# Performance work log

Measured on AMD Instinct MI355X. Metric: run time of the kernel, lower is better.

Reference implementation:

```python
import math
import jax, jax.numpy as jnp
import numpy as np

DIM = 2048
HEAD_DIM = 64
N_HEADS = DIM // HEAD_DIM
BATCH = 4
SEQ = 1025  # 32*32 axial positions + 1 zero position
EPS = 1e-6


def make_theta(head_dim=HEAD_DIM, h=32, w=32):
    # freqs: geometric from pi to 10*pi, head_dim//4 of them
    n_freqs = head_dim // 4
    freqs = jnp.exp(jnp.linspace(math.log(math.pi), math.log(10 * math.pi), n_freqs))
    hp = jnp.linspace(-1.0, 1.0, h + 1)
    wp = jnp.linspace(-1.0, 1.0, w + 1)
    hp = (hp[:-1] + hp[1:]) / 2
    wp = (wp[:-1] + wp[1:]) / 2
    pos = jnp.stack(jnp.meshgrid(hp, wp, indexing='ij'), axis=-1).reshape(h * w, 2)
    pos = jnp.concatenate([jnp.zeros((1, 2)), pos], axis=0)  # [1025, 2]
    theta_h = pos[:, 0:1] * freqs  # [S, n_freqs]
    theta_w = pos[:, 1:2] * freqs
    return jnp.concatenate([theta_h, theta_w], axis=-1)  # [S, head_dim//2]


def rms_norm(x, scale, eps=EPS):
    mean_sq = jnp.mean(jnp.square(x.astype(jnp.float32)), axis=-1, keepdims=True)
    s = scale.astype(jnp.float32) * jax.lax.rsqrt(mean_sq + eps)
    return (x * s.astype(x.dtype)).astype(x.dtype)


def apply_rotary(x, theta):
    # x: [B, H, S, D], theta: [S, d] with 2*d <= D
    d = theta.shape[-1]
    x1, x2, x3 = x[..., :d], x[..., d:2 * d], x[..., 2 * d:]
    cos, sin = jnp.cos(theta), jnp.sin(theta)  # broadcast over B, H
    y1 = x1 * cos - x2 * sin
    y2 = x2 * cos + x1 * sin
    return jnp.concatenate([y1, y2, x3], axis=-1)


def setup_inputs() -> dict:
    key = jax.random.key(0)
    k1, k2, k3 = jax.random.split(key, 3)
    x = jax.random.normal(k1, (BATCH, SEQ, DIM), dtype=jnp.float32)
    scale = jnp.ones((DIM,), dtype=jnp.float32)
    w_qkv = jax.random.normal(k2, (3 * DIM, DIM), dtype=jnp.float32) * 0.02
    w_out = jax.random.normal(k3, (DIM, DIM), dtype=jnp.float32) * 0.02
    return {"x": x, "scale": scale, "w_qkv": w_qkv, "w_out": w_out}


def reference(x, scale, w_qkv, w_out):
    B, S, _ = x.shape
    skip = x
    h = rms_norm(x, scale)
    qkv = h @ w_qkv.T  # [B, S, 3*DIM]
    qkv = qkv.reshape(B, S, 3, N_HEADS, HEAD_DIM)
    qkv = jnp.transpose(qkv, (0, 3, 2, 1, 4))  # [B, H, 3, S, D]
    q, k, v = qkv[:, :, 0], qkv[:, :, 1], qkv[:, :, 2]
    theta = make_theta()[:S]
    q = apply_rotary(q, theta)
    k = apply_rotary(k, theta)
    scores = jnp.einsum('bhqd,bhkd->bhqk', q, k) / math.sqrt(HEAD_DIM)
    causal = jnp.tril(jnp.ones((S, S), dtype=bool))
    scores = jnp.where(causal, scores, jnp.finfo(scores.dtype).min)
    attn = jax.nn.softmax(scores, axis=-1)
    o = jnp.einsum('bhqk,bhkd->bhqd', attn, v)  # [B, H, S, D]
    o = jnp.transpose(o, (0, 2, 1, 3)).reshape(B, S, DIM)
    return o @ w_out.T + skip
```

## Files before the change

kernel.cpp:

```cpp
#include <hip/hip_runtime.h>
#include <hip/hip_bf16.h>
#include <cstdint>

#define SEQ   1025
#define SPAD  1088
#define DIM   2048
#define NQKV  6144
#define MROWS 4100
#define MPAD  4352
#define NH    32

typedef __attribute__((ext_vector_type(8))) short bf16x8;
typedef __attribute__((ext_vector_type(4))) short bf16x4;
typedef __attribute__((ext_vector_type(4))) float f32x4;

#define MFMA16x16(A,B,C) __builtin_amdgcn_mfma_f32_16x16x32_bf16(A,B,C,0,0,0)

static __device__ __forceinline__ float bf2f(short s) {
    union { unsigned int u; float f; } v;
    v.u = ((unsigned int)(unsigned short)s) << 16;
    return v.f;
}
static __device__ __forceinline__ short f2bf(float f) {
    union { float f; unsigned int u; } v; v.f = f;
    unsigned int r = v.u + 0x7fffu + ((v.u >> 16) & 1u);
    return (short)(r >> 16);
}

typedef __attribute__((address_space(1))) unsigned int u32g;
typedef __attribute__((address_space(3))) unsigned int u32l;
static __device__ __forceinline__ void gld_lds16(void* lds, const void* g) {
    __builtin_amdgcn_global_load_lds((const u32g*)(uintptr_t)g,
                                     (u32l*)(uintptr_t)lds, 16, 0, 0);
}

#define SBX() __builtin_amdgcn_sched_barrier(0)
#define PRIO(x) __builtin_amdgcn_s_setprio(x)
#define VMCNT(n) asm volatile("s_waitcnt vmcnt(" #n ")" ::: "memory")
#define LGKM(n)  asm volatile("s_waitcnt lgkmcnt(" #n ")" ::: "memory")

__global__ __launch_bounds__(256) void prep_k(const float* __restrict__ x,
        const float* __restrict__ sc, short* __restrict__ h,
        const float* __restrict__ wq, short* __restrict__ wqb,
        const float* __restrict__ wo, short* __restrict__ wob,
        float* __restrict__ cosT, float* __restrict__ sinT) {
    __shared__ float red[4];
    int blk = blockIdx.x, t = threadIdx.x;
    if (blk < MPAD) {
        int row = blk;
        short* hr = h + (size_t)row * DIM;
        if (row >= MROWS) {
            bf16x8 z = {};
            *(bf16x8*)(hr + t*8) = z;
            return;
        }
        const float4* xr = (const float4*)(x + (size_t)row * DIM);
        float4 a = xr[2*t], b2 = xr[2*t+1];
        float ss = a.x*a.x + a.y*a.y + a.z*a.z + a.w*a.w
                 + b2.x*b2.x + b2.y*b2.y + b2.z*b2.z + b2.w*b2.w;
        #pragma unroll
        for (int off = 32; off; off >>= 1) ss += __shfl_xor(ss, off, 64);
        if ((t & 63) == 0) red[t >> 6] = ss;
        __syncthreads();
        float ms = (red[0]+red[1]+red[2]+red[3]) * (1.0f/2048.0f);
        float inv = rsqrtf(ms + 1e-6f);
        const float4* sr = (const float4*)sc;
        float4 s0 = sr[2*t], s1 = sr[2*t+1];
        bf16x8 o;
        o[0]=f2bf(a.x*(s0.x*inv));  o[1]=f2bf(a.y*(s0.y*inv));
        o[2]=f2bf(a.z*(s0.z*inv));  o[3]=f2bf(a.w*(s0.w*inv));
        o[4]=f2bf(b2.x*(s1.x*inv)); o[5]=f2bf(b2.y*(s1.y*inv));
        o[6]=f2bf(b2.z*(s1.z*inv)); o[7]=f2bf(b2.w*(s1.w*inv));
        *(bf16x8*)(hr + t*8) = o;
        return;
    }
    blk -= MPAD;
    constexpr int N4A = NQKV*DIM/4;
    constexpr int N4B = DIM*DIM/4;
    constexpr int NCB = (N4A + N4B + 255)/256;
    if (blk < NCB) {
        int i = blk*256 + t;
        const float* src; short* dst; int j;
        if (i < N4A) { src = wq; dst = wqb; j = i; }
        else { j = i - N4A; if (j >= N4B) return; src = wo; dst = wob; }
        float4 v = ((const float4*)src)[j];
        bf16x4 r = { f2bf(v.x), f2bf(v.y), f2bf(v.z), f2bf(v.w) };
        *(bf16x4*)(dst + (size_t)j*4) = r;
        return;
    }
    blk -= NCB;
    int i = blk*256 + t;
    if (i >= SEQ * 16) return;
    int s = i >> 4, f = i & 15;
    float ph = 0.f, pw = 0.f;
    if (s > 0) {
        int p = s - 1;
        ph = -1.f + ((p >> 5) + 0.5f) * 0.0625f;
        pw = -1.f + ((p & 31) + 0.5f) * 0.0625f;
    }
    double fr = 3.141592653589793 * exp((double)f * 0.15350567286626973);
    float th = (float)(ph * fr), tw = (float)(pw * fr);
    cosT[s*32 + f]      = cosf(th);
    sinT[s*32 + f]      = sinf(th);
    cosT[s*32 + 16 + f] = cosf(tw);
    sinT[s*32 + 16 + f] = sinf(tw);
}

template<int EPI>
__global__ __launch_bounds__(512, 2) void gemm8p(const short* __restrict__ A,
                                                 const short* __restrict__ B,
                                                 void* __restrict__ C,
                                                 const float* __restrict__ skip,
                                                 int N, int K, int nbm) {
    extern __shared__ char smem[];
    const int nwg = gridDim.x;
    const int cpx = nwg >> 3;
    const int bid = blockIdx.x;
    const int sid = (bid & 7) * cpx + (bid >> 3);
    const int bm = sid % nbm;
    const int bn = sid / nbm;

    const int t = threadIdx.x, w = t >> 6, l = t & 63;
    const int lr = l & 15, lg = l >> 4;
    const int wr = w >> 2, wc = w & 3;

    const short* Ab = A + (size_t)bm * 256 * K;
    const short* Bb = B + (size_t)bn * 256 * K;

    const int srow = t >> 3;
    const int scol = (((t & 7) ^ (srow & 7)) << 3);

    const int cs0 = (lg * 16) ^ ((lr & 7) << 4);
    const int cs1 = (64 + lg * 16) ^ ((lr & 7) << 4);
    const int aBase = wr * 16384 + lr * 128;
    const int bBase = 32768 + (wc >> 1) * 16384 + ((wc & 1) * 64 + lr) * 128;

    f32x4 acc[8][4] = {};
    bf16x8 rA[4][2], rB01[2][2], rB23[2][2];

#define STAGE_A(kt, half, bb) do {                                            \
    const int k0_ = (kt) * 64;                                                \
    gld_lds16(smem + (bb)*65536 + (half)*16384 + (w<<10),                     \
              Ab + (size_t)((half)*128 + srow) * K + k0_ + scol);             \
    gld_lds16(smem + (bb)*65536 + (half)*16384 + 8192 + (w<<10),              \
              Ab + (size_t)((half)*128 + 64 + srow) * K + k0_ + scol);        \
} while (0)

#define STAGE_B(kt, half, bb) do {                                            \
    const int k0_ = (kt) * 64;                                                \
    gld_lds16(smem + (bb)*65536 + 32768 + (half)*16384 + (w<<10),             \
              Bb + (size_t)((half)*128 + srow) * K + k0_ + scol);             \
    gld_lds16(smem + (bb)*65536 + 32768 + (half)*16384 + 8192 + (w<<10),      \
              Bb + (size_t)((half)*128 + 64 + srow) * K + k0_ + scol);        \
} while (0)

#define READ_A(bb, h) do {                                                    \
    const char* p_ = smem + (bb)*65536 + aBase + (h)*8192;                    \
    _Pragma("unroll")                                                         \
    for (int am = 0; am < 4; ++am) {                                          \
        rA[am][0] = *(const bf16x8*)(p_ + am*2048 + cs0);                     \
        rA[am][1] = *(const bf16x8*)(p_ + am*2048 + cs1);                     \
    }                                                                         \
} while (0)

#define READ_B(bb, np, arr) do {                                              \
    const char* p_ = smem + (bb)*65536 + bBase + (np)*4096;                   \
    _Pragma("unroll")                                                         \
    for (int nn = 0; nn < 2; ++nn) {                                          \
        arr[nn][0] = *(const bf16x8*)(p_ + nn*2048 + cs0);                    \
        arr[nn][1] = *(const bf16x8*)(p_ + nn*2048 + cs1);                    \
    }                                                                         \
} while (0)

#define MF_Q(h, np, arr) do {                                                 \
    _Pragma("unroll")                                                         \
    for (int am = 0; am < 4; ++am)                                            \
    _Pragma("unroll")                                                         \
    for (int nn = 0; nn < 2; ++nn) {                                          \
        acc[(h)*4+am][(np)*2+nn] =                                            \
            MFMA16x16(rA[am][0], arr[nn][0], acc[(h)*4+am][(np)*2+nn]);       \
        acc[(h)*4+am][(np)*2+nn] =                                            \
            MFMA16x16(rA[am][1], arr[nn][1], acc[(h)*4+am][(np)*2+nn]);       \
    }                                                                         \
} while (0)

#define BOPEN()  do { SBX(); __builtin_amdgcn_s_barrier(); LGKM(0); SBX(); } while (0)
#define BOPEN_NL() do { SBX(); __builtin_amdgcn_s_barrier(); SBX(); } while (0)
#define BCLOSE() do { SBX(); __builtin_amdgcn_s_barrier(); SBX(); } while (0)

    STAGE_B(0, 0, 0); STAGE_B(0, 1, 0);
    STAGE_A(0, 0, 0); STAGE_A(0, 1, 0);
    STAGE_B(1, 0, 1); STAGE_B(1, 1, 1);
    VMCNT(4); SBX();
    __builtin_amdgcn_s_barrier(); SBX();

    const int NT2 = K / 128;
    for (int it = 0; it < NT2; ++it) {
        const bool more = (it < NT2 - 1);
        READ_A(0, 0); READ_B(0, 0, rB01);
        STAGE_A(2*it + 1, 0, 1);
        LGKM(8);
        BOPEN(); PRIO(1); MF_Q(0, 0, rB01); PRIO(0); BCLOSE();
        READ_B(0, 1, rB23);
        STAGE_A(2*it + 1, 1, 1);
        BOPEN(); PRIO(1); MF_Q(0, 1, rB23); PRIO(0); BCLOSE();
        READ_A(0, 1);
        if (more) STAGE_B(2*it + 2, 0, 0);
        BOPEN(); PRIO(1); MF_Q(1, 1, rB23); PRIO(0); BCLOSE();
        if (more) STAGE_B(2*it + 2, 1, 0);
        BOPEN_NL(); PRIO(1); MF_Q(1, 0, rB01); PRIO(0); SBX();
        if (more) { VMCNT(4); } else { VMCNT(0); }
        BCLOSE();
        READ_A(1, 0); READ_B(1, 0, rB01);
        if (more) STAGE_A(2*it + 2, 0, 0);
        LGKM(8);
        BOPEN(); PRIO(1); MF_Q(0, 0, rB01); PRIO(0); BCLOSE();
        READ_B(1, 1, rB23);
        if (more) STAGE_A(2*it + 2, 1, 0);
        BOPEN(); PRIO(1); MF_Q(0, 1, rB23); PRIO(0); BCLOSE();
        READ_A(1, 1);
        if (more) STAGE_B(2*it + 3, 0, 1);
        BOPEN(); PRIO(1); MF_Q(1, 1, rB23); PRIO(0); BCLOSE();
        if (more) STAGE_B(2*it + 3, 1, 1);
        BOPEN_NL(); PRIO(1); MF_Q(1, 0, rB01); PRIO(0); SBX();
        if (more) { VMCNT(4); }
        BCLOSE();
    }

    #pragma unroll
    for (int m = 0; m < 8; ++m) {
        const int row0 = bm*256 + wr*128 + m*16 + lg*4;
        #pragma unroll
        for (int n = 0; n < 4; ++n) {
            const int col = bn*256 + wc*64 + n*16 + lr;
            #pragma unroll
            for (int r = 0; r < 4; ++r) {
                const int row = row0 + r;
                if constexpr (EPI == 0) {
                    ((short*)C)[(size_t)row * N + col] = f2bf(acc[m][n][r]);
                } else {
                    if (row < MROWS)
                        ((float*)C)[(size_t)row * N + col] =
                            acc[m][n][r] + skip[(size_t)row * N + col];
                }
            }
        }
    }
#undef STAGE_A
#undef STAGE_B
#undef READ_A
#undef READ_B
#undef MF_Q
#undef BOPEN
#undef BOPEN_NL
#undef BCLOSE
}

__global__ __launch_bounds__(256) void rearrange_k(const short* __restrict__ qkv,
        const float* __restrict__ cosT, const float* __restrict__ sinT,
        short* __restrict__ kr, short* __restrict__ vt) {
    int bid = blockIdx.x;
    int bh = bid / 17, st = bid % 17;
    int b = bh >> 5, hh = bh & 31;
    int s0 = st * 64;
    int t = threadIdx.x;
    __shared__ short vs[64][68];
    #pragma unroll
    for (int i = 0; i < 8; ++i) {
        int task = t + i*256;
        int sl = task >> 5, p = task & 31;
        int s = s0 + sl;
        float y1 = 0.f, y2 = 0.f;
        if (s < SEQ) {
            const short* src = qkv + (size_t)(b*SEQ + s)*NQKV + DIM + hh*64;
            float x1 = bf2f(src[p]), x2 = bf2f(src[32+p]);
            float c = cosT[s*32+p], sn = sinT[s*32+p];
            y1 = x1*c - x2*sn;
            y2 = x2*c + x1*sn;
        }
        short* dst = kr + ((size_t)bh*SPAD + s)*64;
        dst[p]    = f2bf(y1);
        dst[32+p] = f2bf(y2);
    }
    #pragma unroll
    for (int i = 0; i < 16; ++i) {
        int task = t + i*256;
        int sl = task >> 6, d = task & 63;
        int s = s0 + sl;
        short v = 0;
        if (s < SEQ) v = qkv[(size_t)(b*SEQ + s)*NQKV + 2*DIM + hh*64 + d];
        vs[sl][d] = v;
    }
    __syncthreads();
    #pragma unroll
    for (int i = 0; i < 16; ++i) {
        int task = t + i*256;
        int d = task >> 6, sl = task & 63;
        vt[((size_t)bh*64 + d)*SPAD + s0 + sl] = vs[sl][d];
    }
}

__global__ __launch_bounds__(256) void attn_k(const short* __restrict__ qkv,
        const short* __restrict__ kr, const short* __restrict__ vt,
        const float* __restrict__ cosT, const float* __restrict__ sinT,
        short* __restrict__ ob) {
    const int nwg = gridDim.x;
    const int cpx = nwg >> 3;
    const int bid = blockIdx.x;
    const int sid = (bid & 7) * cpx + (bid >> 3);
    const int bh = sid / 9;
    const int qt = 8 - (sid % 9);
    const int q0 = qt * 128;
    const int b = bh >> 5, hh = bh & 31;
    const int t = threadIdx.x, w = t >> 6, l = t & 63;
    const int lr = l & 15, lg = l >> 4;

    __shared__ short Ks[2][64*64];
    __shared__ short Vts[2][64*64];

    const int qrowA = q0 + w*32 + lr;
    const int qrowB = qrowA + 16;

    bf16x8 qf0A, qf1A, qf0B, qf1B;
    auto loadq = [&](int qrow, bf16x8& f0, bf16x8& f1) {
        int qc = qrow < SEQ ? qrow : SEQ-1;
        const short* qsrc = qkv + (size_t)(b*SEQ + qc)*NQKV + hh*64;
        bf16x8 xlo = *(const bf16x8*)(qsrc + lg*8);
        bf16x8 xhi = *(const bf16x8*)(qsrc + 32 + lg*8);
        float4 c0 = ((const float4*)(cosT + qc*32 + lg*8))[0];
        float4 c1 = ((const float4*)(cosT + qc*32 + lg*8))[1];
        float4 s0 = ((const float4*)(sinT + qc*32 + lg*8))[0];
        float4 s1 = ((const float4*)(sinT + qc*32 + lg*8))[1];
        float cc[8] = {c0.x,c0.y,c0.z,c0.w,c1.x,c1.y,c1.z,c1.w};
        float sn[8] = {s0.x,s0.y,s0.z,s0.w,s1.x,s1.y,s1.z,s1.w};
        #pragma unroll
        for (int j = 0; j < 8; ++j) {
            float x1 = bf2f(xlo[j]), x2 = bf2f(xhi[j]);
            f0[j] = f2bf(x1*cc[j] - x2*sn[j]);
            f1[j] = f2bf(x2*cc[j] + x1*sn[j]);
        }
    };
    loadq(qrowA, qf0A, qf1A);
    loadq(qrowB, qf0B, qf1B);

    f32x4 oaccA[4] = {}, oaccB[4] = {};
    float mrunA = -1e30f, lrunA = 0.f;
    float mrunB = -1e30f, lrunB = 0.f;
    const int ntile = min(2*qt + 2, 17);
    const float SC = 0.125f * 1.4426950408889634f;

    const char* kbase = (const char*)(kr + (size_t)bh * SPAD * 64);
    const char* vbase = (const char*)(vt + (size_t)bh * 64 * SPAD);
    const int srow8 = l >> 3;
    const int sslotB = ((l & 7) ^ srow8) << 4;
    const int swz = (lr & 7) << 4;

#define STAGE_KV(kt_, c) do {                                                  \
    const int kv0_ = (kt_) * 64;                                               \
    gld_lds16((char*)Ks[c] + w*2048,                                           \
              kbase + (size_t)(kv0_ + w*16 + srow8)*128 + sslotB);             \
    gld_lds16((char*)Ks[c] + w*2048 + 1024,                                    \
              kbase + (size_t)(kv0_ + w*16 + 8 + srow8)*128 + sslotB);         \
    gld_lds16((char*)Vts[c] + w*2048,                                          \
              vbase + (size_t)(w*16 + srow8)*(SPAD*2) + (size_t)kv0_*2 + sslotB); \
    gld_lds16((char*)Vts[c] + w*2048 + 1024,                                   \
              vbase + (size_t)(w*16 + 8 + srow8)*(SPAD*2) + (size_t)kv0_*2 + sslotB); \
} while (0)

#define SOFTMAX(st, qrow, pf0, pf1, mrun, lrun, alpha) do {                    \
    float tmax = -1e30f;                                                       \
    _Pragma("unroll")                                                          \
    for (int f = 0; f < 4; ++f)                                                \
    _Pragma("unroll")                                                          \
    for (int r = 0; r < 4; ++r) {                                              \
        int kv = kv0 + f*16 + lg*4 + r;                                        \
        float v = st[f][r] * SC;                                               \
        v = (kv <= (qrow) && kv < SEQ) ? v : -1e30f;                           \
        st[f][r] = v; tmax = fmaxf(tmax, v);                                   \
    }                                                                          \
    tmax = fmaxf(tmax, __shfl_xor(tmax, 16, 64));                              \
    tmax = fmaxf(tmax, __shfl_xor(tmax, 32, 64));                              \
    float mnew = fmaxf(mrun, tmax);                                            \
    alpha = exp2f(mrun - mnew);                                                \
    float psum = 0.f;                                                          \
    _Pragma("unroll")                                                          \
    for (int j = 0; j < 4; ++j) {                                              \
        float p0 = exp2f(st[0][j] - mnew);                                     \
        float p1 = exp2f(st[1][j] - mnew);                                     \
        float p2 = exp2f(st[2][j] - mnew);                                     \
        float p3 = exp2f(st[3][j] - mnew);                                     \
        psum += (p0 + p1) + (p2 + p3);                                         \
        pf0[j] = f2bf(p0); pf0[4+j] = f2bf(p1);                                \
        pf1[j] = f2bf(p2); pf1[4+j] = f2bf(p3);                                \
    }                                                                          \
    psum += __shfl_xor(psum, 16, 64);                                          \
    psum += __shfl_xor(psum, 32, 64);                                          \
    lrun = lrun * alpha + psum;                                                \
    mrun = mnew;                                                               \
} while (0)

    STAGE_KV(0, 0);

    for (int kt = 0; kt < ntile; ++kt) {
        const int kv0 = kt * 64;
        const int cur = kt & 1;
        if (kt + 1 < ntile) { STAGE_KV(kt + 1, cur ^ 1); SBX(); VMCNT(4); }
        else { SBX(); VMCNT(0); }
        SBX(); __builtin_amdgcn_s_barrier(); SBX();

        f32x4 stA[4], stB[4];
        #pragma unroll
        for (int f = 0; f < 4; ++f) {
            const char* kp = (const char*)Ks[cur] + (f*16 + lr)*128;
            bf16x8 a0 = *(const bf16x8*)(kp + ((lg*16) ^ swz));
            bf16x8 a1 = *(const bf16x8*)(kp + ((64 + lg*16) ^ swz));
            f32x4 zA = {};
            zA = MFMA16x16(a0, qf0A, zA);
            stA[f] = MFMA16x16(a1, qf1A, zA);
            f32x4 zB = {};
            zB = MFMA16x16(a0, qf0B, zB);
            stB[f] = MFMA16x16(a1, qf1B, zB);
        }

        bf16x8 pfA0, pfA1, pfB0, pfB1;
        float alphaA, alphaB;
        SOFTMAX(stA, qrowA, pfA0, pfA1, mrunA, lrunA, alphaA);
        SOFTMAX(stB, qrowB, pfB0, pfB1, mrunB, lrunB, alphaB);

        #pragma unroll
        for (int df = 0; df < 4; ++df) {
            oaccA[df][0] *= alphaA; oaccA[df][1] *= alphaA;
            oaccA[df][2] *= alphaA; oaccA[df][3] *= alphaA;
            oaccB[df][0] *= alphaB; oaccB[df][1] *= alphaB;
            oaccB[df][2] *= alphaB; oaccB[df][3] *= alphaB;
        }

        #pragma unroll
        for (int df = 0; df < 4; ++df) {
            const char* vp = (const char*)Vts[cur] + (df*16 + lr)*128;
            bf16x4 v0 = *(const bf16x4*)(vp + ((lg*8) ^ swz));
            bf16x4 v1 = *(const bf16x4*)(vp + ((32 + lg*8) ^ swz));
            bf16x4 v2 = *(const bf16x4*)(vp + ((64 + lg*8) ^ swz));
            bf16x4 v3 = *(const bf16x4*)(vp + ((96 + lg*8) ^ swz));
            bf16x8 vf0, vf1;
            vf0[0]=v0[0]; vf0[1]=v0[1]; vf0[2]=v0[2]; vf0[3]=v0[3];
            vf0[4]=v1[0]; vf0[5]=v1[1]; vf0[6]=v1[2]; vf0[7]=v1[3];
            vf1[0]=v2[0]; vf1[1]=v2[1]; vf1[2]=v2[2]; vf1[3]=v2[3];
            vf1[4]=v3[0]; vf1[5]=v3[1]; vf1[6]=v3[2]; vf1[7]=v3[3];
            oaccA[df] = MFMA16x16(vf0, pfA0, oaccA[df]);
            oaccA[df] = MFMA16x16(vf1, pfA1, oaccA[df]);
            oaccB[df] = MFMA16x16(vf0, pfB0, oaccB[df]);
            oaccB[df] = MFMA16x16(vf1, pfB1, oaccB[df]);
        }
        SBX(); __builtin_amdgcn_s_barrier(); SBX();
    }
#undef STAGE_KV
#undef SOFTMAX

    auto writeo = [&](int qrow, const f32x4* oacc, float lrun) {
        if (qrow < SEQ) {
            float inv = 1.0f / lrun;
            short* orow = ob + (size_t)(b*SEQ + qrow)*DIM + hh*64;
            #pragma unroll
            for (int df = 0; df < 4; ++df) {
                bf16x4 ov = { f2bf(oacc[df][0]*inv), f2bf(oacc[df][1]*inv),
                              f2bf(oacc[df][2]*inv), f2bf(oacc[df][3]*inv) };
                *(bf16x4*)(orow + df*16 + lg*4) = ov;
            }
        }
    };
    writeo(qrowA, oaccA, lrunA);
    writeo(qrowB, oaccB, lrunB);
}

extern "C" void kernel_launch(void* const* d_in, const int* in_sizes, int n_in,
                              void* d_out, int out_size, void* d_ws, size_t ws_size,
                              hipStream_t stream) {
    const float* x     = (const float*)d_in[0];
    const float* scale = (const float*)d_in[1];
    const float* w_qkv = (const float*)d_in[2];
    const float* w_out = (const float*)d_in[3];
    float* out = (float*)d_out;

    char* ws = (char*)d_ws;
    size_t off = 0;
    auto alloc = [&](size_t bytes) -> char* {
        char* p = ws + off;
        off += (bytes + 255) & ~(size_t)255;
        return p;
    };
    float* cosT  = (float*)alloc((size_t)SEQ*32*4);
    float* sinT  = (float*)alloc((size_t)SEQ*32*4);
    short* h_b   = (short*)alloc((size_t)MPAD*DIM*2);
    short* wq_b  = (short*)alloc((size_t)NQKV*DIM*2);
    short* wo_b  = (short*)alloc((size_t)DIM*DIM*2);
    short* qkv_b = (short*)alloc((size_t)MPAD*NQKV*2);
    short* k_r   = (short*)alloc((size_t)128*SPAD*64*2);
    short* vt    = (short*)alloc((size_t)128*SPAD*64*2);
    short* o_b   = h_b;

    hipFuncSetAttribute((const void*)gemm8p<0>,
                        hipFuncAttributeMaxDynamicSharedMemorySize, 131072);
    hipFuncSetAttribute((const void*)gemm8p<1>,
                        hipFuncAttributeMaxDynamicSharedMemorySize, 131072);

    constexpr int NCB = (NQKV*DIM/4 + DIM*DIM/4 + 255)/256;
    prep_k<<<MPAD + NCB + 65, 256, 0, stream>>>(x, scale, h_b,
                                                w_qkv, wq_b, w_out, wo_b, cosT, sinT);
    gemm8p<0><<<(MPAD/256)*(NQKV/256), 512, 131072, stream>>>(h_b, wq_b, qkv_b, nullptr, NQKV, DIM, MPAD/256);
    rearrange_k<<<128*17, 256, 0, stream>>>(qkv_b, cosT, sinT, k_r, vt);
    attn_k<<<128*9, 256, 0, stream>>>(qkv_b, k_r, vt, cosT, sinT, o_b);
    gemm8p<1><<<(MPAD/256)*(DIM/256), 512, 131072, stream>>>(o_b, wo_b, out, x, DIM, DIM, MPAD/256);
}
```

Baseline: 450.5 us.

## Fuse rotary embedding and K/V rearrangement into QKV GEMM epilogue

Removes the separate rearrange kernel and the rotary step in the attention prologue. The QKV GEMM epilogue now applies rotary to Q and K using an interleaved cos/sin table, writes Q densely, writes K in per-head padded layout, and writes V transposed. The intent is to avoid writing and re-reading the full QKV intermediate and to drop one launch. The block-to-tile mapping is also changed so each XCD handles a contiguous range of N tiles. In exchange, the V store becomes a strided 2-byte scatter, and padded K/V rows past SEQ are no longer zeroed, which could leave uninitialized workspace values in those rows.

```diff
diff --git a/kernel.cpp b/kernel.cpp
--- a/kernel.cpp
+++ b/kernel.cpp
@@ -43,7 +43,7 @@
         const float* __restrict__ sc, short* __restrict__ h,
         const float* __restrict__ wq, short* __restrict__ wqb,
         const float* __restrict__ wo, short* __restrict__ wob,
-        float* __restrict__ cosT, float* __restrict__ sinT) {
+        float2* __restrict__ csT) {
     __shared__ float red[4];
     int blk = blockIdx.x, t = threadIdx.x;
     if (blk < MPAD) {
@@ -100,10 +100,8 @@
     }
     double fr = 3.141592653589793 * exp((double)f * 0.15350567286626973);
     float th = (float)(ph * fr), tw = (float)(pw * fr);
-    cosT[s*32 + f]      = cosf(th);
-    sinT[s*32 + f]      = sinf(th);
-    cosT[s*32 + 16 + f] = cosf(tw);
-    sinT[s*32 + 16 + f] = sinf(tw);
+    csT[s*32 + f]      = make_float2(cosf(th), sinf(th));
+    csT[s*32 + 16 + f] = make_float2(cosf(tw), sinf(tw));
 }
 
 template<int EPI>
@@ -111,14 +109,17 @@
                                                  const short* __restrict__ B,
                                                  void* __restrict__ C,
                                                  const float* __restrict__ skip,
-                                                 int N, int K, int nbm) {
+                                                 short* __restrict__ qout,
+                                                 short* __restrict__ kout,
+                                                 short* __restrict__ vout,
+                                                 const float2* __restrict__ csT,
+                                                 int N, int K, int nbm, int nbn) {
     extern __shared__ char smem[];
-    const int nwg = gridDim.x;
-    const int cpx = nwg >> 3;
     const int bid = blockIdx.x;
-    const int sid = (bid & 7) * cpx + (bid >> 3);
-    const int bm = sid % nbm;
-    const int bn = sid / nbm;
+    const int xcd = bid & 7, local = bid >> 3;
+    const int bnper = nbn >> 3;
+    const int bm = local / bnper;
+    const int bn = xcd * bnper + (local - bm * bnper);
 
     const int t = threadIdx.x, w = t >> 6, l = t & 63;
     const int lr = l & 15, lg = l >> 4;
@@ -227,18 +228,54 @@
         BCLOSE();
     }
 
-    #pragma unroll
-    for (int m = 0; m < 8; ++m) {
-        const int row0 = bm*256 + wr*128 + m*16 + lg*4;
-        #pragma unroll
-        for (int n = 0; n < 4; ++n) {
-            const int col = bn*256 + wc*64 + n*16 + lr;
+    if constexpr (EPI == 0) {
+        const int region = bn >> 3;
+        const int hh = ((bn << 2) | wc) & 31;
+        #pragma unroll
+        for (int m = 0; m < 8; ++m) {
+            const int row0 = bm*256 + wr*128 + m*16 + lg*4;
             #pragma unroll
             for (int r = 0; r < 4; ++r) {
                 const int row = row0 + r;
-                if constexpr (EPI == 0) {
-                    ((short*)C)[(size_t)row * N + col] = f2bf(acc[m][n][r]);
+                if (row >= MROWS) continue;
+                const int b_ = row / SEQ;
+                const int s_ = row - b_ * SEQ;
+                if (region == 0) {
+                    short* qr = qout + (size_t)row * DIM + bn*256 + wc*64;
+                    #pragma unroll
+                    for (int n = 0; n < 2; ++n) {
+                        float2 cs = csT[s_*32 + n*16 + lr];
+                        float x1 = acc[m][n][r], x2 = acc[m][n+2][r];
+                        qr[n*16 + lr]     = f2bf(x1*cs.x - x2*cs.y);
+                        qr[(n+2)*16 + lr] = f2bf(x2*cs.x + x1*cs.y);
+                    }
+                } else if (region == 1) {
+                    short* kr_ = kout + ((size_t)(b_*NH + hh)*SPAD + s_)*64;
+                    #pragma unroll
+                    for (int n = 0; n < 2; ++n) {
+                        float2 cs = csT[s_*32 + n*16 + lr];
+                        float x1 = acc[m][n][r], x2 = acc[m][n+2][r];
+                        kr_[n*16 + lr]     = f2bf(x1*cs.x - x2*cs.y);
+                        kr_[(n+2)*16 + lr] = f2bf(x2*cs.x + x1*cs.y);
+                    }
                 } else {
+                    #pragma unroll
+                    for (int n = 0; n < 4; ++n)
+                        vout[((size_t)(b_*NH + hh)*64 + n*16 + lr)*SPAD + s_]
+                            = f2bf(acc[m][n][r]);
+                }
+            }
+        }
+    } else {
+        #pragma unroll
+        for (int m = 0; m < 8; ++m) {
+            const int row0 = bm*256 + wr*128 + m*16 + lg*4;
+            #pragma unroll
+            for (int n = 0; n < 4; ++n) {
+                const int col = bn*256 + wc*64 + n*16 + lr;
+                #pragma unroll
+                for (int r = 0; r < 4; ++r) {
+                    const int row = row0 + r;
                     if (row < MROWS)
                         ((float*)C)[(size_t)row * N + col] =
                             acc[m][n][r] + skip[(size_t)row * N + col];
@@ -256,53 +293,8 @@
 #undef BCLOSE
 }
 
-__global__ __launch_bounds__(256) void rearrange_k(const short* __restrict__ qkv,
-        const float* __restrict__ cosT, const float* __restrict__ sinT,
-        short* __restrict__ kr, short* __restrict__ vt) {
-    int bid = blockIdx.x;
-    int bh = bid / 17, st = bid % 17;
-    int b = bh >> 5, hh = bh & 31;
-    int s0 = st * 64;
-    int t = threadIdx.x;
-    __shared__ short vs[64][68];
-    #pragma unroll
-    for (int i = 0; i < 8; ++i) {
-        int task = t + i*256;
-        int sl = task >> 5, p = task & 31;
-        int s = s0 + sl;
-        float y1 = 0.f, y2 = 0.f;
-        if (s < SEQ) {
-            const short* src = qkv + (size_t)(b*SEQ + s)*NQKV + DIM + hh*64;
-            float x1 = bf2f(src[p]), x2 = bf2f(src[32+p]);
-            float c = cosT[s*32+p], sn = sinT[s*32+p];
-            y1 = x1*c - x2*sn;
-            y2 = x2*c + x1*sn;
-        }
-        short* dst = kr + ((size_t)bh*SPAD + s)*64;
-        dst[p]    = f2bf(y1);
-        dst[32+p] = f2bf(y2);
-    }
-    #pragma unroll
-    for (int i = 0; i < 16; ++i) {
-        int task = t + i*256;
-        int sl = task >> 6, d = task & 63;
-        int s = s0 + sl;
-        short v = 0;
-        if (s < SEQ) v = qkv[(size_t)(b*SEQ + s)*NQKV + 2*DIM + hh*64 + d];
-        vs[sl][d] = v;
-    }
-    __syncthreads();
-    #pragma unroll
-    for (int i = 0; i < 16; ++i) {
-        int task = t + i*256;
-        int d = task >> 6, sl = task & 63;
-        vt[((size_t)bh*64 + d)*SPAD + s0 + sl] = vs[sl][d];
-    }
-}
-
-__global__ __launch_bounds__(256) void attn_k(const short* __restrict__ qkv,
+__global__ __launch_bounds__(256) void attn_k(const short* __restrict__ qb,
         const short* __restrict__ kr, const short* __restrict__ vt,
-        const float* __restrict__ cosT, const float* __restrict__ sinT,
         short* __restrict__ ob) {
     const int nwg = gridDim.x;
     const int cpx = nwg >> 3;
@@ -322,26 +314,16 @@
     const int qrowB = qrowA + 16;
 
     bf16x8 qf0A, qf1A, qf0B, qf1B;
-    auto loadq = [&](int qrow, bf16x8& f0, bf16x8& f1) {
-        int qc = qrow < SEQ ? qrow : SEQ-1;
-        const short* qsrc = qkv + (size_t)(b*SEQ + qc)*NQKV + hh*64;
-        bf16x8 xlo = *(const bf16x8*)(qsrc + lg*8);
-        bf16x8 xhi = *(const bf16x8*)(qsrc + 32 + lg*8);
-        float4 c0 = ((const float4*)(cosT + qc*32 + lg*8))[0];
-        float4 c1 = ((const float4*)(cosT + qc*32 + lg*8))[1];
-        float4 s0 = ((const float4*)(sinT + qc*32 + lg*8))[0];
-        float4 s1 = ((const float4*)(sinT + qc*32 + lg*8))[1];
-        float cc[8] = {c0.x,c0.y,c0.z,c0.w,c1.x,c1.y,c1.z,c1.w};
-        float sn[8] = {s0.x,s0.y,s0.z,s0.w,s1.x,s1.y,s1.z,s1.w};
-        #pragma unroll
-        for (int j = 0; j < 8; ++j) {
-            float x1 = bf2f(xlo[j]), x2 = bf2f(xhi[j]);
-            f0[j] = f2bf(x1*cc[j] - x2*sn[j]);
-            f1[j] = f2bf(x2*cc[j] + x1*sn[j]);
-        }
-    };
-    loadq(qrowA, qf0A, qf1A);
-    loadq(qrowB, qf0B, qf1B);
+    {
+        int qcA = qrowA < SEQ ? qrowA : SEQ-1;
+        int qcB = qrowB < SEQ ? qrowB : SEQ-1;
+        const short* qsA = qb + ((size_t)b*SEQ + qcA)*DIM + hh*64;
+        const short* qsB = qb + ((size_t)b*SEQ + qcB)*DIM + hh*64;
+        qf0A = *(const bf16x8*)(qsA + lg*8);
+        qf1A = *(const bf16x8*)(qsA + 32 + lg*8);
+        qf0B = *(const bf16x8*)(qsB + lg*8);
+        qf1B = *(const bf16x8*)(qsB + 32 + lg*8);
+    }
 
     f32x4 oaccA[4] = {}, oaccB[4] = {};
     float mrunA = -1e30f, lrunA = 0.f;
@@ -489,12 +471,11 @@
         off += (bytes + 255) & ~(size_t)255;
         return p;
     };
-    float* cosT  = (float*)alloc((size_t)SEQ*32*4);
-    float* sinT  = (float*)alloc((size_t)SEQ*32*4);
+    float2* csT  = (float2*)alloc((size_t)SEQ*32*8);
     short* h_b   = (short*)alloc((size_t)MPAD*DIM*2);
     short* wq_b  = (short*)alloc((size_t)NQKV*DIM*2);
     short* wo_b  = (short*)alloc((size_t)DIM*DIM*2);
-    short* qkv_b = (short*)alloc((size_t)MPAD*NQKV*2);
+    short* q_b   = (short*)alloc((size_t)MPAD*DIM*2);
     short* k_r   = (short*)alloc((size_t)128*SPAD*64*2);
     short* vt    = (short*)alloc((size_t)128*SPAD*64*2);
     short* o_b   = h_b;
@@ -506,9 +487,10 @@
 
     constexpr int NCB = (NQKV*DIM/4 + DIM*DIM/4 + 255)/256;
     prep_k<<<MPAD + NCB + 65, 256, 0, stream>>>(x, scale, h_b,
-                                                w_qkv, wq_b, w_out, wo_b, cosT, sinT);
-    gemm8p<0><<<(MPAD/256)*(NQKV/256), 512, 131072, stream>>>(h_b, wq_b, qkv_b, nullptr, NQKV, DIM, MPAD/256);
-    rearrange_k<<<128*17, 256, 0, stream>>>(qkv_b, cosT, sinT, k_r, vt);
-    attn_k<<<128*9, 256, 0, stream>>>(qkv_b, k_r, vt, cosT, sinT, o_b);
-    gemm8p<1><<<(MPAD/256)*(DIM/256), 512, 131072, stream>>>(o_b, wo_b, out, x, DIM, DIM, MPAD/256);
-}
+                                                w_qkv, wq_b, w_out, wo_b, csT);
+    gemm8p<0><<<(MPAD/256)*(NQKV/256), 512, 131072, stream>>>(
+        h_b, wq_b, nullptr, nullptr, q_b, k_r, vt, csT, NQKV, DIM, MPAD/256, NQKV/256);
+    attn_k<<<128*9, 256, 0, stream>>>(q_b, k_r, vt, o_b);
+    gemm8p<1><<<(MPAD/256)*(DIM/256), 512, 131072, stream>>>(
+        o_b, wo_b, out, x, nullptr, nullptr, nullptr, nullptr, DIM, DIM, MPAD/256, DIM/256);
+}
```

Result: slower. 467.9 us (+3.9%).
